# Performance work log

Hardware: AMD Instinct MI355X
Metric: run time of the kernel (lower is better)

Reference implementation:

```python
import jax, jax.numpy as jnp
import numpy as np

# Config (decoder-only Transformer)
NL, H, D, DK, V, B, S = 6, 16, 1024, 64, 32000, 2, 1024  # DK = d_v = D // H
DFF = 4 * D


def _layer_norm(x, g, b, eps=1e-5):
    mu = jnp.mean(x, axis=-1, keepdims=True)
    var = jnp.mean(jnp.square(x - mu), axis=-1, keepdims=True)
    return (x - mu) * jax.lax.rsqrt(var + eps) * g + b


def _pos_encoding(seq_len, d_embed):
    # Matches PositionalEncoding: base 1000 (as in source), sin at even i, cos at odd i
    pos = jnp.arange(seq_len, dtype=jnp.float32)[:, None]
    i = jnp.arange(d_embed, dtype=jnp.float32)[None, :]
    angle = pos / jnp.power(1000.0, i / d_embed)
    return jnp.where((jnp.arange(d_embed)[None, :] % 2) == 0, jnp.sin(angle), jnp.cos(angle))


def setup_inputs() -> dict:
    key = jax.random.key(0)
    ks = jax.random.split(key, 8)
    n = lambda k, shp, sc: jax.random.normal(k, shp, dtype=jnp.float32) * sc
    return {
        "outputs": jax.random.randint(ks[0], (B, S), 0, V),
        "embed": n(ks[1], (V, D), 0.02),
        # per-head Q/K/V projections stacked over layers and heads: [NL, H, D, DK]
        "Wq": n(ks[2], (NL, H, D, DK), D ** -0.5),
        "Wk": n(ks[3], (NL, H, D, DK), D ** -0.5),
        "Wv": n(ks[4], (NL, H, D, DK), D ** -0.5),
        "W1": n(ks[5], (NL, D, DFF), D ** -0.5),
        "W2": n(ks[6], (NL, DFF, D), DFF ** -0.5),
        "ln1_g": jnp.ones((NL, D), jnp.float32),
        "ln1_b": jnp.zeros((NL, D), jnp.float32),
        "ln2_g": jnp.ones((NL, D), jnp.float32),
        "ln2_b": jnp.zeros((NL, D), jnp.float32),
        "Wout": n(ks[7], (D, V), D ** -0.5),
        "bout": jnp.zeros((V,), jnp.float32),
    }


def reference(outputs, embed, Wq, Wk, Wv, W1, W2, ln1_g, ln1_b, ln2_g, ln2_b, Wout, bout):
    x = embed[outputs]                      # [B, S, D]
    x = x + _pos_encoding(S, D)
    scale = jnp.float32(DK ** 0.5)
    for l in range(NL):
        # Masked multi-head self-attention (per-head projections batched over H)
        q = jnp.einsum('bsd,hdk->bhsk', x, Wq[l])
        k = jnp.einsum('bsd,hdk->bhsk', x, Wk[l])
        v = jnp.einsum('bsd,hdk->bhsk', x, Wv[l])
        scores = jnp.einsum('bhqk,bhsk->bhqs', q, k) / scale   # [B,H,S,S]
        # Faithful to source: tril then masked_fill(score == 0, -inf)
        scores = jnp.tril(scores)
        scores = jnp.where(scores == 0, -jnp.inf, scores)
        w = jax.nn.softmax(scores, axis=-1)
        attn = jnp.einsum('bhqs,bhsv->bqhv', w, v).reshape(B, S, H * DK)
        x = _layer_norm(x + attn, ln1_g[l], ln1_b[l])
        # Position-wise FFN (dropout is identity at inference)
        h = jax.nn.relu(x @ W1[l]) @ W2[l]
        x = _layer_norm(x + h, ln2_g[l], ln2_b[l])
    return x @ Wout + bout                  # logits [B, S, V]
```

## Files before the change

### kernel.cpp

```cpp
#include <hip/hip_runtime.h>

typedef unsigned short u16;
typedef __attribute__((ext_vector_type(8))) short short8;
typedef __attribute__((ext_vector_type(4))) short short4_t;
typedef __attribute__((ext_vector_type(4))) float f32x4;

#define NLAYER 6
#define NH 16
#define DMODEL 1024
#define DHEAD 64
#define NVOCAB 32000
#define NB 2
#define NS 1024
#define NDFF 4096
#define MTOK (NB*NS)

__device__ __forceinline__ u16 f2b(float f) {
    union { float f; unsigned u; } x; x.f = f;
    unsigned r = x.u + 0x7fffu + ((x.u >> 16) & 1u);
    return (u16)(r >> 16);
}

#define GLL16(gp, lp) __builtin_amdgcn_global_load_lds( \
    (const __attribute__((address_space(1))) void*)(gp), \
    (__attribute__((address_space(3))) void*)(lp), 16, 0, 0)

__global__ __launch_bounds__(256) void trans64(
    const float* __restrict__ src, u16* __restrict__ dst,
    int R, int C, long sStride, long dStride)
{
    __shared__ float sh[64][65];
    const int c0 = blockIdx.x * 64, r0 = blockIdx.y * 64;
    const float* s = src + (long)blockIdx.z * sStride;
    u16* d = dst + (long)blockIdx.z * dStride;
    const int tid = threadIdx.x;
    const int lr = tid >> 4, lc = (tid & 15) * 4;
    #pragma unroll
    for (int q = 0; q < 4; ++q) {
        const float4 v = *(const float4*)(s + (long)(r0 + q * 16 + lr) * C + c0 + lc);
        sh[q * 16 + lr][lc + 0] = v.x;
        sh[q * 16 + lr][lc + 1] = v.y;
        sh[q * 16 + lr][lc + 2] = v.z;
        sh[q * 16 + lr][lc + 3] = v.w;
    }
    __syncthreads();
    #pragma unroll
    for (int k = 0; k < 2; ++k) {
        const int t = tid + 256 * k;
        const int col = t >> 3, rch = (t & 7) * 8;
        u16 tmp[8];
        #pragma unroll
        for (int j = 0; j < 8; ++j) tmp[j] = f2b(sh[rch + j][col]);
        *(short8*)(d + (long)(c0 + col) * R + r0 + rch) = *(const short8*)tmp;
    }
}

__global__ void transpose_qkv(const float* __restrict__ src, u16* __restrict__ dst, int sel)
{
    __shared__ float t[32][33];
    const int bi = blockIdx.z, l = bi >> 4, h = bi & 15;
    const float* s = src + (long)bi * (DMODEL * DHEAD);
    u16* d = dst + (long)l * 3072 * DMODEL + (long)(sel * 1024 + h * 64) * DMODEL;
    const int c0 = blockIdx.x * 32, r0 = blockIdx.y * 32;
    const int tx = threadIdx.x, ty = threadIdx.y;
    #pragma unroll
    for (int j = 0; j < 32; j += 8)
        t[ty + j][tx] = s[(long)(r0 + ty + j) * DHEAD + c0 + tx];
    __syncthreads();
    #pragma unroll
    for (int j = 0; j < 32; j += 8)
        d[(long)(c0 + ty + j) * DMODEL + r0 + tx] = f2b(t[tx][ty + j]);
}

__global__ void embed_pe(const int* __restrict__ toks, const float* __restrict__ emb,
                         float* __restrict__ x, u16* __restrict__ xb)
{
    const int row = blockIdx.x;
    const int s = row & (NS - 1);
    const long erow = (long)toks[row] * DMODEL;
    const long base = (long)row * DMODEL;
    #pragma unroll
    for (int j = 0; j < 4; ++j) {
        int d = threadIdx.x + j * 256;
        float ang = (float)s * exp2f(-(float)d * (9.965784284662087f / 1024.f));
        float pe = (d & 1) ? cosf(ang) : sinf(ang);
        float v = emb[erow + d] + pe;
        x[base + d] = v;
        xb[base + d] = f2b(v);
    }
}

template<int ND>
__global__ __launch_bounds__(256) void ln_residual(
    const float* __restrict__ xin, const float* __restrict__ delta, size_t pstride,
    const float* __restrict__ g, const float* __restrict__ bb,
    float* __restrict__ xout, u16* __restrict__ xbout)
{
    __shared__ float red[8];
    const long base = (long)blockIdx.x * DMODEL;
    const int d = threadIdx.x * 4;
    f32x4 v = *(const f32x4*)(xin + base + d);
    #pragma unroll
    for (int y = 0; y < ND; ++y)
        v += *(const f32x4*)(delta + base + (size_t)y * pstride + d);
    float sum = v[0] + v[1] + v[2] + v[3];
    float sq  = v[0]*v[0] + v[1]*v[1] + v[2]*v[2] + v[3]*v[3];
    #pragma unroll
    for (int off = 1; off < 64; off <<= 1) {
        sum += __shfl_xor(sum, off, 64);
        sq  += __shfl_xor(sq,  off, 64);
    }
    const int wv = threadIdx.x >> 6, lane = threadIdx.x & 63;
    if (lane == 0) { red[wv] = sum; red[4 + wv] = sq; }
    __syncthreads();
    float ts = red[0] + red[1] + red[2] + red[3];
    float tq = red[4] + red[5] + red[6] + red[7];
    float mu = ts * (1.f / DMODEL);
    float var = tq * (1.f / DMODEL) - mu * mu;
    float rstd = rsqrtf(var + 1e-5f);
    const f32x4 gg = *(const f32x4*)(g + d);
    const f32x4 bv = *(const f32x4*)(bb + d);
    f32x4 yv = (v - mu) * rstd * gg + bv;
    *(f32x4*)(xout + base + d) = yv;
    u16 fourv[4];
    #pragma unroll
    for (int i = 0; i < 4; ++i) fourv[i] = f2b(yv[i]);
    *(short4_t*)(xbout + base + d) = *(const short4_t*)fourv;
}

template<int BM, int EPI>
__global__ __launch_bounds__(BM*2, 2) void gemm_pipe(
    const u16* __restrict__ A, const u16* __restrict__ Bt,
    void* __restrict__ Cout, const float* __restrict__ bias,
    int M, int N, int K, int lda, int ldb, size_t zstride)
{
    constexpr int WAVES = BM / 32;
    constexpr int WC = WAVES / 2;
    constexpr int MR = BM / 32;
    constexpr int TILE = BM * 32;

    __shared__ __align__(16) u16 As[4][TILE];
    __shared__ __align__(16) u16 Bs[4][TILE];

    const int nmb = M / BM;
    const int id = blockIdx.x, nwg = gridDim.x;
    const int q = nwg >> 3, r = nwg & 7, xcd = id & 7, loc = id >> 3;
    const int swz = (xcd < r ? xcd * (q + 1) : r * (q + 1) + (xcd - r) * q) + loc;
    const int m0 = (swz % nmb) * BM, n0 = (swz / nmb) * BM;
    const int koff = blockIdx.y * K;

    const int tid = threadIdx.x, wv = tid >> 6, lane = tid & 63;
    const int wr = wv / WC, wc = wv % WC;
    const int lrow = lane & 15, ks = lane >> 4;

    const u16* gsrc[4];
    int ldso[2];
    {
        const int l4 = lane >> 2, s = lane & 3;
        #pragma unroll
        for (int j = 0; j < 2; ++j) {
            const int row = j * (WAVES * 16) + wv * 16 + l4;
            const int x = (row >> 1) & 3;
            gsrc[j]     = A  + (size_t)(m0 + row) * lda + koff + (size_t)((s ^ x) * 8);
            gsrc[2 + j] = Bt + (size_t)(n0 + row) * ldb + koff + (size_t)((s ^ x) * 8);
            ldso[j] = (j * (WAVES * 16) + wv * 16) * 32;
        }
    }
    int aoff[MR], boff[4];
    #pragma unroll
    for (int m = 0; m < MR; ++m) {
        const int row = wr * (BM / 2) + m * 16 + lrow;
        aoff[m] = row * 32 + ((ks ^ ((row >> 1) & 3)) * 8);
    }
    #pragma unroll
    for (int n = 0; n < 4; ++n) {
        const int row = wc * 64 + n * 16 + lrow;
        boff[n] = row * 32 + ((ks ^ ((row >> 1) & 3)) * 8);
    }

    const int NT = K / 32;
    auto ISSUE = [&](int t) {
        const int b = t & 3;
        const size_t ko = (size_t)t * 32;
        #pragma unroll
        for (int j = 0; j < 2; ++j) {
            GLL16(gsrc[j] + ko,     &As[b][ldso[j]]);
            GLL16(gsrc[2 + j] + ko, &Bs[b][ldso[j]]);
        }
    };

    f32x4 acc[MR][4] = {};
    ISSUE(0); ISSUE(1); ISSUE(2);

    for (int t = 0; t < NT; ++t) {
        if (t < NT - 2)       { asm volatile("s_waitcnt vmcnt(8)" ::: "memory"); }
        else if (t == NT - 2) { asm volatile("s_waitcnt vmcnt(4)" ::: "memory"); }
        else                  { asm volatile("s_waitcnt vmcnt(0)" ::: "memory"); }
        __builtin_amdgcn_sched_barrier(0);
        __builtin_amdgcn_s_barrier();
        __builtin_amdgcn_sched_barrier(0);

        const int b = t & 3;
        short8 af[MR], bf[4];
        #pragma unroll
        for (int m = 0; m < MR; ++m) af[m] = *(const short8*)(&As[b][aoff[m]]);
        #pragma unroll
        for (int n = 0; n < 4; ++n)  bf[n] = *(const short8*)(&Bs[b][boff[n]]);
        if (t + 3 < NT) ISSUE(t + 3);
        __builtin_amdgcn_s_setprio(1);
        #pragma unroll
        for (int m = 0; m < MR; ++m)
            #pragma unroll
            for (int n = 0; n < 4; ++n)
                acc[m][n] = __builtin_amdgcn_mfma_f32_16x16x32_bf16(af[m], bf[n], acc[m][n], 0, 0, 0);
        __builtin_amdgcn_s_setprio(0);
    }

    if (EPI == 0 || EPI == 3) {
        __syncthreads();
        float* patch = (float*)((WAVES == 8 && (wv & 4)) ? (void*)&Bs[0][0] : (void*)&As[0][0])
                       + (wv & 3) * (16 * 68);
        const int cc0 = n0 + wc * 64;
        f32x4 bvv = {};
        if (EPI == 3) bvv = *(const f32x4*)(bias + cc0 + (lane & 15) * 4);
        float* C = (float*)Cout + (EPI == 0 ? (size_t)blockIdx.y * zstride : (size_t)0);
        #pragma unroll
        for (int m = 0; m < MR; ++m) {
            #pragma unroll
            for (int n = 0; n < 4; ++n)
                #pragma unroll
                for (int i = 0; i < 4; ++i)
                    patch[(ks * 4 + i) * 68 + n * 16 + lrow] = acc[m][n][i];
            #pragma unroll
            for (int i2 = 0; i2 < 4; ++i2) {
                const int prow = i2 * 4 + ks;
                f32x4 v = *(const f32x4*)(patch + prow * 68 + (lane & 15) * 4);
                if (EPI == 3) v += bvv;
                const int rr = m0 + wr * (BM / 2) + m * 16 + prow;
                *(f32x4*)(C + (size_t)rr * N + cc0 + (lane & 15) * 4) = v;
            }
        }
    } else {
        u16* C = (u16*)Cout;
        #pragma unroll
        for (int m = 0; m < MR; ++m) {
            const int rr = m0 + wr * (BM / 2) + m * 16 + ks * 4;
            #pragma unroll
            for (int n = 0; n < 4; ++n) {
                const int cc = n0 + wc * 64 + n * 16 + lrow;
                #pragma unroll
                for (int i = 0; i < 4; ++i) {
                    float vv = acc[m][n][i];
                    if (EPI == 2) vv = fmaxf(vv, 0.f);
                    C[(size_t)(rr + i) * N + cc] = f2b(vv);
                }
            }
        }
    }
}

__global__ __launch_bounds__(256, 2) void attn_flash4(
    const u16* __restrict__ qk, const u16* __restrict__ vT, float* __restrict__ delta)
{
    __shared__ __align__(16) u16 Qs[64 * 64];
    __shared__ __align__(16) u16 Kd[2][64 * 64];
    __shared__ __align__(16) u16 Vd[2][64 * 64];
    __shared__ __align__(16) u16 Ps[4][16 * 64];

    const int pair = blockIdx.x, h = blockIdx.y, b = blockIdx.z;
    const int tid = threadIdx.x, wv = tid >> 6, lane = tid & 63;
    const int lrow = lane & 15, ks4 = lane >> 4, li4 = ks4 * 4;
    const long baseQK = (long)b * NS * 2048;
    const u16* vbase = vT + (long)h * 64 * 2048 + b * NS;
    u16* ps = &Ps[wv][0];

    for (int rep = 0; rep < 2; ++rep) {
        const int qt = rep ? 15 - pair : pair;
        __syncthreads();

        #pragma unroll
        for (int i = 0; i < 2; ++i) {
            const int c = (wv * 2 + i) * 64 + lane;
            const int row = c >> 3, u = (c & 7) ^ (row & 7);
            GLL16(qk + baseQK + (long)(qt * 64 + row) * 2048 + h * 64 + u * 8, Qs + c * 8);
            GLL16(qk + baseQK + (long)row * 2048 + 1024 + h * 64 + u * 8, Kd[0] + c * 8);
            GLL16(vbase + (long)row * 2048 + u * 8, Vd[0] + c * 8);
        }
        __syncthreads();

        short8 aq[2];
        {
            const int row = wv * 16 + lrow;
            aq[0] = *(const short8*)(Qs + row * 64 + ((ks4 ^ (row & 7)) * 8));
            aq[1] = *(const short8*)(Qs + row * 64 + (((4 + ks4) ^ (row & 7)) * 8));
        }

        f32x4 o[4] = {};
        float m_ = -__builtin_inff(), l_ = 0.f;

        for (int t = 0; t <= qt; ++t) {
            const int p = t & 1;
            if (t < qt) {
                #pragma unroll
                for (int i = 0; i < 2; ++i) {
                    const int c = (wv * 2 + i) * 64 + lane;
                    const int row = c >> 3, u = (c & 7) ^ (row & 7);
                    GLL16(qk + baseQK + (long)((t + 1) * 64 + row) * 2048 + 1024 + h * 64 + u * 8, Kd[p ^ 1] + c * 8);
                    GLL16(vbase + (long)row * 2048 + (t + 1) * 64 + u * 8, Vd[p ^ 1] + c * 8);
                }
            }
            f32x4 sa[4];
            #pragma unroll
            for (int nb = 0; nb < 4; ++nb) {
                f32x4 z = {};
                #pragma unroll
                for (int kd = 0; kd < 2; ++kd) {
                    const int row = nb * 16 + lrow;
                    short8 bk = *(const short8*)(Kd[p] + row * 64 + (((kd * 4 + ks4) ^ (row & 7)) * 8));
                    z = __builtin_amdgcn_mfma_f32_16x16x32_bf16(bk, aq[kd], z, 0, 0, 0);
                }
                sa[nb] = z;
            }
            const int qg = qt * 64 + wv * 16 + lrow;
            #pragma unroll
            for (int nb = 0; nb < 4; ++nb)
                #pragma unroll
                for (int i = 0; i < 4; ++i) {
                    float sc = sa[nb][i] * 0.125f;
                    if (t == qt && (t * 64 + nb * 16 + li4 + i) > qg) sc = -__builtin_inff();
                    sa[nb][i] = sc;
                }
            float mt = sa[0][0];
            #pragma unroll
            for (int nb = 0; nb < 4; ++nb)
                #pragma unroll
                for (int i = 0; i < 4; ++i) mt = fmaxf(mt, sa[nb][i]);
            mt = fmaxf(mt, __shfl_xor(mt, 16, 64));
            mt = fmaxf(mt, __shfl_xor(mt, 32, 64));
            const float mn = fmaxf(m_, mt);
            const float fac = expf(m_ - mn);
            m_ = mn;
            float rs = 0.f;
            #pragma unroll
            for (int nb = 0; nb < 4; ++nb)
                #pragma unroll
                for (int i = 0; i < 4; ++i) {
                    float pp = expf(sa[nb][i] - mn);
                    sa[nb][i] = pp; rs += pp;
                }
            rs += __shfl_xor(rs, 16, 64);
            rs += __shfl_xor(rs, 32, 64);
            l_ = l_ * fac + rs;
            #pragma unroll
            for (int nd = 0; nd < 4; ++nd) o[nd] *= fac;

            #pragma unroll
            for (int nb = 0; nb < 4; ++nb) {
                u16 fourv[4];
                #pragma unroll
                for (int i = 0; i < 4; ++i) fourv[i] = f2b(sa[nb][i]);
                const int kvb = nb * 16 + li4;
                const int addr = lrow * 64 + (((kvb >> 3) ^ (lrow & 7)) * 8) + (kvb & 7);
                *(short4_t*)(ps + addr) = *(const short4_t*)fourv;
            }
            short8 pa[2];
            pa[0] = *(const short8*)(ps + lrow * 64 + ((ks4 ^ (lrow & 7)) * 8));
            pa[1] = *(const short8*)(ps + lrow * 64 + (((4 + ks4) ^ (lrow & 7)) * 8));
            #pragma unroll
            for (int nd = 0; nd < 4; ++nd)
                #pragma unroll
                for (int kd = 0; kd < 2; ++kd) {
                    const int row = nd * 16 + lrow;
                    short8 vb = *(const short8*)(Vd[p] + row * 64 + (((kd * 4 + ks4) ^ (row & 7)) * 8));
                    o[nd] = __builtin_amdgcn_mfma_f32_16x16x32_bf16(vb, pa[kd], o[nd], 0, 0, 0);
                }
            __syncthreads();
        }

        const float inv = 1.f / l_;
        const long tok = (long)b * NS + qt * 64 + wv * 16 + lrow;
        #pragma unroll
        for (int nd = 0; nd < 4; ++nd) {
            f32x4 v = o[nd] * inv;
            *(f32x4*)(delta + tok * DMODEL + h * 64 + nd * 16 + li4) = v;
        }
    }
}

extern "C" void kernel_launch(void* const* d_in, const int* in_sizes, int n_in,
                              void* d_out, int out_size, void* d_ws, size_t ws_size,
                              hipStream_t stream) {
    const int*   toks  = (const int*)d_in[0];
    const float* emb   = (const float*)d_in[1];
    const float* Wq    = (const float*)d_in[2];
    const float* Wk    = (const float*)d_in[3];
    const float* Wv    = (const float*)d_in[4];
    const float* W1    = (const float*)d_in[5];
    const float* W2    = (const float*)d_in[6];
    const float* ln1g  = (const float*)d_in[7];
    const float* ln1b  = (const float*)d_in[8];
    const float* ln2g  = (const float*)d_in[9];
    const float* ln2b  = (const float*)d_in[10];
    const float* Wout  = (const float*)d_in[11];
    const float* bout  = (const float*)d_in[12];

    char* p = (char*)d_ws;
    auto alloc = [&](size_t bytes) { void* r = (void*)p; p += (bytes + 255) & ~(size_t)255; return r; };
    const size_t PSZ = (size_t)MTOK * 1024;
    u16*   Wqkv_t = (u16*)alloc((size_t)NLAYER * 3072 * 1024 * 2);
    u16*   W1t    = (u16*)alloc((size_t)NLAYER * 4096 * 1024 * 2);
    u16*   W2t    = (u16*)alloc((size_t)NLAYER * 1024 * 4096 * 2);
    u16*   Woutt  = (u16*)alloc((size_t)NVOCAB * 1024 * 2);
    float* x      = (float*)alloc((size_t)MTOK * 1024 * 4);
    u16*   xb     = (u16*)alloc((size_t)MTOK * 1024 * 2);
    u16*   qkbuf  = (u16*)alloc((size_t)MTOK * 2048 * 2);
    u16*   vTbuf  = (u16*)alloc((size_t)1024 * MTOK * 2);
    u16*   hbuf   = (u16*)alloc((size_t)MTOK * 4096 * 2);
    float* dbuf   = (float*)alloc(PSZ * 4 * 4);

    float* hbufF = (float*)hbuf;

    transpose_qkv<<<dim3(2, 32, 96), dim3(32, 8), 0, stream>>>(Wq, Wqkv_t, 0);
    transpose_qkv<<<dim3(2, 32, 96), dim3(32, 8), 0, stream>>>(Wk, Wqkv_t, 1);
    transpose_qkv<<<dim3(2, 32, 96), dim3(32, 8), 0, stream>>>(Wv, Wqkv_t, 2);
    trans64<<<dim3(64, 16, 6), 256, 0, stream>>>(W1, W1t, 1024, 4096, 1024l * 4096, 4096l * 1024);
    trans64<<<dim3(16, 64, 6), 256, 0, stream>>>(W2, W2t, 4096, 1024, 4096l * 1024, 1024l * 4096);
    trans64<<<dim3(500, 16, 1), 256, 0, stream>>>(Wout, Woutt, 1024, NVOCAB, 0, 0);

    embed_pe<<<MTOK, 256, 0, stream>>>(toks, emb, x, xb);

    for (int l = 0; l < NLAYER; ++l) {
        const u16* Wl = Wqkv_t + (size_t)l * 3072 * 1024;
        gemm_pipe<128, 1><<<dim3(16 * 16), 256, 0, stream>>>(
            xb, Wl, qkbuf, nullptr, MTOK, 2048, 1024, 1024, 1024, 0);
        gemm_pipe<128, 1><<<dim3(8 * 16), 256, 0, stream>>>(
            Wl + (size_t)2048 * 1024, xb, vTbuf, nullptr, 1024, MTOK, 1024, 1024, 1024, 0);
        attn_flash4<<<dim3(8, NH, NB), 256, 0, stream>>>(qkbuf, vTbuf, hbufF);
        ln_residual<1><<<MTOK, 256, 0, stream>>>(x, hbufF, 0,
            ln1g + l * 1024, ln1b + l * 1024, x, xb);
        gemm_pipe<128, 2><<<dim3(16 * 32), 256, 0, stream>>>(
            xb, W1t + (size_t)l * 4096 * 1024, hbuf, nullptr, MTOK, 4096, 1024, 1024, 1024, 0);
        gemm_pipe<128, 0><<<dim3(16 * 8, 4), 256, 0, stream>>>(
            hbuf, W2t + (size_t)l * 1024 * 4096, dbuf, nullptr, MTOK, 1024, 1024, 4096, 4096, PSZ);
        ln_residual<4><<<MTOK, 256, 0, stream>>>(x, dbuf, PSZ,
            ln2g + l * 1024, ln2b + l * 1024, x, xb);
    }

    gemm_pipe<256, 3><<<dim3(8 * 125), 512, 0, stream>>>(
        xb, Woutt, (float*)d_out, bout, MTOK, NVOCAB, 1024, 1024, 1024, 0);
}
```

Baseline: 1.158 ms.

## Switch GEMM MFMA to 32x32x16 tiles and halve W2 split-K partials

The pipelined GEMM now issues 32x32x16 bf16 MFMA instructions instead of 16x16x32 ones, with new LDS fragment offsets and rewritten epilogue index mappings for the 16-element accumulators. This is meant to cut LDS fragment reads per MFMA and raise matrix-core efficiency. Separately, the FFN down-projection split-K factor drops from 4 to 2, which halves the partial-sum buffer traffic and the reduction work in the following layernorm. The cost is fewer workgroups for that GEMM, so occupancy is lower there.

```diff
diff --git a/kernel.cpp b/kernel.cpp
--- a/kernel.cpp
+++ b/kernel.cpp
@@ -4,6 +4,7 @@
 typedef __attribute__((ext_vector_type(8))) short short8;
 typedef __attribute__((ext_vector_type(4))) short short4_t;
 typedef __attribute__((ext_vector_type(4))) float f32x4;
+typedef __attribute__((ext_vector_type(16))) float f32x16;
 
 #define NLAYER 6
 #define NH 16
@@ -136,7 +137,7 @@
 {
     constexpr int WAVES = BM / 32;
     constexpr int WC = WAVES / 2;
-    constexpr int MR = BM / 32;
+    constexpr int MT = (BM / 2) / 32;
     constexpr int TILE = BM * 32;
 
     __shared__ __align__(16) u16 As[4][TILE];
@@ -151,7 +152,7 @@
 
     const int tid = threadIdx.x, wv = tid >> 6, lane = tid & 63;
     const int wr = wv / WC, wc = wv % WC;
-    const int lrow = lane & 15, ks = lane >> 4;
+    const int l31 = lane & 31, kh = lane >> 5;
 
     const u16* gsrc[4];
     int ldso[2];
@@ -166,17 +167,21 @@
             ldso[j] = (j * (WAVES * 16) + wv * 16) * 32;
         }
     }
-    int aoff[MR], boff[4];
-    #pragma unroll
-    for (int m = 0; m < MR; ++m) {
-        const int row = wr * (BM / 2) + m * 16 + lrow;
-        aoff[m] = row * 32 + ((ks ^ ((row >> 1) & 3)) * 8);
-    }
-    #pragma unroll
-    for (int n = 0; n < 4; ++n) {
-        const int row = wc * 64 + n * 16 + lrow;
-        boff[n] = row * 32 + ((ks ^ ((row >> 1) & 3)) * 8);
-    }
+    int aoff[MT][2], boff[2][2];
+    #pragma unroll
+    for (int mt = 0; mt < MT; ++mt)
+        #pragma unroll
+        for (int kk = 0; kk < 2; ++kk) {
+            const int row = wr * (BM / 2) + mt * 32 + l31;
+            aoff[mt][kk] = row * 32 + (((kk * 2 + kh) ^ ((row >> 1) & 3)) * 8);
+        }
+    #pragma unroll
+    for (int nt = 0; nt < 2; ++nt)
+        #pragma unroll
+        for (int kk = 0; kk < 2; ++kk) {
+            const int row = wc * 64 + nt * 32 + l31;
+            boff[nt][kk] = row * 32 + (((kk * 2 + kh) ^ ((row >> 1) & 3)) * 8);
+        }
 
     const int NT = K / 32;
     auto ISSUE = [&](int t) {
@@ -189,7 +194,7 @@
         }
     };
 
-    f32x4 acc[MR][4] = {};
+    f32x16 acc[MT][2] = {};
     ISSUE(0); ISSUE(1); ISSUE(2);
 
     for (int t = 0; t < NT; ++t) {
@@ -201,58 +206,65 @@
         __builtin_amdgcn_sched_barrier(0);
 
         const int b = t & 3;
-        short8 af[MR], bf[4];
-        #pragma unroll
-        for (int m = 0; m < MR; ++m) af[m] = *(const short8*)(&As[b][aoff[m]]);
-        #pragma unroll
-        for (int n = 0; n < 4; ++n)  bf[n] = *(const short8*)(&Bs[b][boff[n]]);
+        short8 af[MT][2], bf[2][2];
+        #pragma unroll
+        for (int mt = 0; mt < MT; ++mt)
+            #pragma unroll
+            for (int kk = 0; kk < 2; ++kk) af[mt][kk] = *(const short8*)(&As[b][aoff[mt][kk]]);
+        #pragma unroll
+        for (int nt = 0; nt < 2; ++nt)
+            #pragma unroll
+            for (int kk = 0; kk < 2; ++kk) bf[nt][kk] = *(const short8*)(&Bs[b][boff[nt][kk]]);
         if (t + 3 < NT) ISSUE(t + 3);
         __builtin_amdgcn_s_setprio(1);
         #pragma unroll
-        for (int m = 0; m < MR; ++m)
-            #pragma unroll
-            for (int n = 0; n < 4; ++n)
-                acc[m][n] = __builtin_amdgcn_mfma_f32_16x16x32_bf16(af[m], bf[n], acc[m][n], 0, 0, 0);
+        for (int mt = 0; mt < MT; ++mt)
+            #pragma unroll
+            for (int nt = 0; nt < 2; ++nt)
+                #pragma unroll
+                for (int kk = 0; kk < 2; ++kk)
+                    acc[mt][nt] = __builtin_amdgcn_mfma_f32_32x32x16_bf16(
+                        af[mt][kk], bf[nt][kk], acc[mt][nt], 0, 0, 0);
         __builtin_amdgcn_s_setprio(0);
     }
 
     if (EPI == 0 || EPI == 3) {
         __syncthreads();
-        float* patch = (float*)((WAVES == 8 && (wv & 4)) ? (void*)&Bs[0][0] : (void*)&As[0][0])
-                       + (wv & 3) * (16 * 68);
+        float* patch = (float*)((wv & WC) ? (void*)&Bs[0][0] : (void*)&As[0][0])
+                       + (wv & (WC - 1)) * (32 * 68);
+        float* C = (float*)Cout + (EPI == 0 ? (size_t)blockIdx.y * zstride : (size_t)0);
         const int cc0 = n0 + wc * 64;
         f32x4 bvv = {};
         if (EPI == 3) bvv = *(const f32x4*)(bias + cc0 + (lane & 15) * 4);
-        float* C = (float*)Cout + (EPI == 0 ? (size_t)blockIdx.y * zstride : (size_t)0);
-        #pragma unroll
-        for (int m = 0; m < MR; ++m) {
-            #pragma unroll
-            for (int n = 0; n < 4; ++n)
-                #pragma unroll
-                for (int i = 0; i < 4; ++i)
-                    patch[(ks * 4 + i) * 68 + n * 16 + lrow] = acc[m][n][i];
-            #pragma unroll
-            for (int i2 = 0; i2 < 4; ++i2) {
-                const int prow = i2 * 4 + ks;
+        #pragma unroll
+        for (int mt = 0; mt < MT; ++mt) {
+            #pragma unroll
+            for (int nt = 0; nt < 2; ++nt)
+                #pragma unroll
+                for (int rg = 0; rg < 16; ++rg)
+                    patch[((rg & 3) + 8 * (rg >> 2) + 4 * kh) * 68 + nt * 32 + l31] = acc[mt][nt][rg];
+            #pragma unroll
+            for (int i2 = 0; i2 < 8; ++i2) {
+                const int prow = i2 * 4 + (lane >> 4);
                 f32x4 v = *(const f32x4*)(patch + prow * 68 + (lane & 15) * 4);
                 if (EPI == 3) v += bvv;
-                const int rr = m0 + wr * (BM / 2) + m * 16 + prow;
+                const int rr = m0 + wr * (BM / 2) + mt * 32 + prow;
                 *(f32x4*)(C + (size_t)rr * N + cc0 + (lane & 15) * 4) = v;
             }
         }
     } else {
         u16* C = (u16*)Cout;
         #pragma unroll
-        for (int m = 0; m < MR; ++m) {
-            const int rr = m0 + wr * (BM / 2) + m * 16 + ks * 4;
-            #pragma unroll
-            for (int n = 0; n < 4; ++n) {
-                const int cc = n0 + wc * 64 + n * 16 + lrow;
-                #pragma unroll
-                for (int i = 0; i < 4; ++i) {
-                    float vv = acc[m][n][i];
+        for (int mt = 0; mt < MT; ++mt) {
+            const int rbase = m0 + wr * (BM / 2) + mt * 32 + 4 * kh;
+            #pragma unroll
+            for (int nt = 0; nt < 2; ++nt) {
+                const int cc = n0 + wc * 64 + nt * 32 + l31;
+                #pragma unroll
+                for (int rg = 0; rg < 16; ++rg) {
+                    float vv = acc[mt][nt][rg];
                     if (EPI == 2) vv = fmaxf(vv, 0.f);
-                    C[(size_t)(rr + i) * N + cc] = f2b(vv);
+                    C[(size_t)(rbase + (rg & 3) + 8 * (rg >> 2)) * N + cc] = f2b(vv);
                 }
             }
         }
@@ -416,7 +428,7 @@
     u16*   qkbuf  = (u16*)alloc((size_t)MTOK * 2048 * 2);
     u16*   vTbuf  = (u16*)alloc((size_t)1024 * MTOK * 2);
     u16*   hbuf   = (u16*)alloc((size_t)MTOK * 4096 * 2);
-    float* dbuf   = (float*)alloc(PSZ * 4 * 4);
+    float* dbuf   = (float*)alloc(PSZ * 2 * 4);
 
     float* hbufF = (float*)hbuf;
 
@@ -440,9 +452,9 @@
             ln1g + l * 1024, ln1b + l * 1024, x, xb);
         gemm_pipe<128, 2><<<dim3(16 * 32), 256, 0, stream>>>(
             xb, W1t + (size_t)l * 4096 * 1024, hbuf, nullptr, MTOK, 4096, 1024, 1024, 1024, 0);
-        gemm_pipe<128, 0><<<dim3(16 * 8, 4), 256, 0, stream>>>(
-            hbuf, W2t + (size_t)l * 1024 * 4096, dbuf, nullptr, MTOK, 1024, 1024, 4096, 4096, PSZ);
-        ln_residual<4><<<MTOK, 256, 0, stream>>>(x, dbuf, PSZ,
+        gemm_pipe<128, 0><<<dim3(16 * 8, 2), 256, 0, stream>>>(
+            hbuf, W2t + (size_t)l * 1024 * 4096, dbuf, nullptr, MTOK, 1024, 2048, 4096, 4096, PSZ);
+        ln_residual<2><<<MTOK, 256, 0, stream>>>(x, dbuf, PSZ,
             ln2g + l * 1024, ln2b + l * 1024, x, xb);
     }
 
```

Result: slower. 1.194 ms (+3.2%).

## Add 8-phase pipelined 256x256 GEMM for output projection; halve FFN2 split-K

Applied to the files above, without the earlier changes.

Adds a new gemm8p kernel for the vocab projection. It uses 256x256 tiles, XCD-aware block swizzling, and a double-buffered LDS pipeline that interleaves global-to-LDS loads with four MFMA phases per k-tile, using setprio and explicit waitcnt control. Separately, the FFN down-projection split-K goes from 4 to 2 partials, which cuts partial-sum traffic and the reduction work in ln_residual at the cost of fewer workgroups. The new kernel's hand-tuned barrier and wait scheduling is fragile and raises register and LDS pressure.

```diff
diff --git a/kernel.cpp b/kernel.cpp
--- a/kernel.cpp
+++ b/kernel.cpp
@@ -255,6 +255,163 @@
                     C[(size_t)(rr + i) * N + cc] = f2b(vv);
                 }
             }
+        }
+    }
+}
+
+__global__ __launch_bounds__(512, 2) void gemm8p(
+    const u16* __restrict__ A, const u16* __restrict__ Bt,
+    float* __restrict__ C, const float* __restrict__ bias,
+    int M, int N, int K)
+{
+    __shared__ __align__(16) u16 As[2][2][128 * 64];
+    __shared__ __align__(16) u16 Bs[2][2][128 * 64];
+
+    const int nmb = M >> 8;
+    const int id = blockIdx.x, nwg = gridDim.x;
+    const int q = nwg >> 3, r = nwg & 7, xcd = id & 7, loc = id >> 3;
+    const int swz = (xcd < r ? xcd * (q + 1) : r * (q + 1) + (xcd - r) * q) + loc;
+    const int m0 = (swz % nmb) * 256, n0 = (swz / nmb) * 256;
+
+    const int tid = threadIdx.x, wv = tid >> 6, lane = tid & 63;
+    const int wr = wv >> 2, wc = wv & 3, bh = wc >> 1;
+    const int lrow = lane & 15, ks4 = lane >> 4;
+
+    const u16* sA[2][2]; const u16* sB[2][2]; int dso[2];
+    #pragma unroll
+    for (int i = 0; i < 2; ++i) {
+        const int c = tid + i * 512, row = c >> 3, pp = c & 7;
+        const int uc = (pp ^ (row & 7)) * 8;
+        #pragma unroll
+        for (int h = 0; h < 2; ++h) {
+            sA[i][h] = A  + (size_t)(m0 + h * 128 + row) * K + uc;
+            sB[i][h] = Bt + (size_t)(n0 + h * 128 + row) * K + uc;
+        }
+        dso[i] = c * 8;
+    }
+    int aoff[8][2], boff[4][2];
+    #pragma unroll
+    for (int m = 0; m < 8; ++m) {
+        const int hr = m * 16 + lrow;
+        #pragma unroll
+        for (int kk = 0; kk < 2; ++kk)
+            aoff[m][kk] = hr * 64 + (((kk * 4 + ks4) ^ (hr & 7)) * 8);
+    }
+    #pragma unroll
+    for (int n = 0; n < 4; ++n) {
+        const int hr = (wc & 1) * 64 + n * 16 + lrow;
+        #pragma unroll
+        for (int kk = 0; kk < 2; ++kk)
+            boff[n][kk] = hr * 64 + (((kk * 4 + ks4) ^ (hr & 7)) * 8);
+    }
+
+    auto SA_ = [&](int t, int h) {
+        const int s = t & 1; const size_t ko = (size_t)t * 64;
+        #pragma unroll
+        for (int i = 0; i < 2; ++i) GLL16(sA[i][h] + ko, &As[s][h][dso[i]]);
+    };
+    auto SB_ = [&](int t, int h) {
+        const int s = t & 1; const size_t ko = (size_t)t * 64;
+        #pragma unroll
+        for (int i = 0; i < 2; ++i) GLL16(sB[i][h] + ko, &Bs[s][h][dso[i]]);
+    };
+
+    const int NT = K >> 6;
+    SB_(0, 0); SB_(0, 1); SA_(0, 0); SA_(0, 1); SB_(1, 0);
+
+    f32x4 acc[8][4] = {};
+    short8 af[4], bf[4];
+
+    for (int t = 0; t < NT; ++t) {
+        const int s = t & 1;
+        if (t < NT - 1) { asm volatile("s_waitcnt vmcnt(2)" ::: "memory"); }
+        else            { asm volatile("s_waitcnt vmcnt(0)" ::: "memory"); }
+        __builtin_amdgcn_sched_barrier(0);
+        __builtin_amdgcn_s_barrier();
+        __builtin_amdgcn_sched_barrier(0);
+
+        #pragma unroll
+        for (int m = 0; m < 4; ++m) af[m] = *(const short8*)(&As[s][wr][aoff[m][0]]);
+        #pragma unroll
+        for (int n = 0; n < 4; ++n) bf[n] = *(const short8*)(&Bs[s][bh][boff[n][0]]);
+        if (t + 1 < NT) SB_(t + 1, 1);
+        __builtin_amdgcn_s_barrier();
+        asm volatile("s_waitcnt lgkmcnt(0)" ::: "memory");
+        __builtin_amdgcn_sched_barrier(0);
+        __builtin_amdgcn_s_setprio(1);
+        #pragma unroll
+        for (int m = 0; m < 4; ++m)
+            #pragma unroll
+            for (int n = 0; n < 4; ++n)
+                acc[m][n] = __builtin_amdgcn_mfma_f32_16x16x32_bf16(af[m], bf[n], acc[m][n], 0, 0, 0);
+        __builtin_amdgcn_s_setprio(0);
+        __builtin_amdgcn_s_barrier();
+
+        #pragma unroll
+        for (int m = 0; m < 4; ++m) af[m] = *(const short8*)(&As[s][wr][aoff[4 + m][0]]);
+        if (t + 1 < NT) SA_(t + 1, 0);
+        __builtin_amdgcn_s_barrier();
+        asm volatile("s_waitcnt lgkmcnt(0)" ::: "memory");
+        __builtin_amdgcn_sched_barrier(0);
+        __builtin_amdgcn_s_setprio(1);
+        #pragma unroll
+        for (int m = 0; m < 4; ++m)
+            #pragma unroll
+            for (int n = 0; n < 4; ++n)
+                acc[4 + m][n] = __builtin_amdgcn_mfma_f32_16x16x32_bf16(af[m], bf[n], acc[4 + m][n], 0, 0, 0);
+        __builtin_amdgcn_s_setprio(0);
+        __builtin_amdgcn_s_barrier();
+
+        #pragma unroll
+        for (int m = 0; m < 4; ++m) af[m] = *(const short8*)(&As[s][wr][aoff[m][1]]);
+        #pragma unroll
+        for (int n = 0; n < 4; ++n) bf[n] = *(const short8*)(&Bs[s][bh][boff[n][1]]);
+        if (t + 1 < NT) SA_(t + 1, 1);
+        __builtin_amdgcn_s_barrier();
+        asm volatile("s_waitcnt lgkmcnt(0)" ::: "memory");
+        __builtin_amdgcn_sched_barrier(0);
+        __builtin_amdgcn_s_setprio(1);
+        #pragma unroll
+        for (int m = 0; m < 4; ++m)
+            #pragma unroll
+            for (int n = 0; n < 4; ++n)
+                acc[m][n] = __builtin_amdgcn_mfma_f32_16x16x32_bf16(af[m], bf[n], acc[m][n], 0, 0, 0);
+        __builtin_amdgcn_s_setprio(0);
+        __builtin_amdgcn_s_barrier();
+
+        #pragma unroll
+        for (int m = 0; m < 4; ++m) af[m] = *(const short8*)(&As[s][wr][aoff[4 + m][1]]);
+        if (t + 2 < NT) SB_(t + 2, 0);
+        __builtin_amdgcn_s_barrier();
+        asm volatile("s_waitcnt lgkmcnt(0)" ::: "memory");
+        __builtin_amdgcn_sched_barrier(0);
+        __builtin_amdgcn_s_setprio(1);
+        #pragma unroll
+        for (int m = 0; m < 4; ++m)
+            #pragma unroll
+            for (int n = 0; n < 4; ++n)
+                acc[4 + m][n] = __builtin_amdgcn_mfma_f32_16x16x32_bf16(af[m], bf[n], acc[4 + m][n], 0, 0, 0);
+        __builtin_amdgcn_s_setprio(0);
+    }
+
+    __syncthreads();
+    float* patch = (float*)((wv & 4) ? (void*)&Bs[0][0][0] : (void*)&As[0][0][0])
+                   + (wv & 3) * (16 * 68);
+    const int cc0 = n0 + wc * 64;
+    const f32x4 bvv = *(const f32x4*)(bias + cc0 + (lane & 15) * 4);
+    #pragma unroll
+    for (int m = 0; m < 8; ++m) {
+        #pragma unroll
+        for (int n = 0; n < 4; ++n)
+            #pragma unroll
+            for (int i = 0; i < 4; ++i)
+                patch[(ks4 * 4 + i) * 68 + n * 16 + lrow] = acc[m][n][i];
+        #pragma unroll
+        for (int i2 = 0; i2 < 4; ++i2) {
+            const int prow = i2 * 4 + ks4;
+            f32x4 v = *(const f32x4*)(patch + prow * 68 + (lane & 15) * 4) + bvv;
+            const int rr = m0 + wr * 128 + m * 16 + prow;
+            *(f32x4*)(C + (size_t)rr * N + cc0 + (lane & 15) * 4) = v;
         }
     }
 }
@@ -416,7 +573,7 @@
     u16*   qkbuf  = (u16*)alloc((size_t)MTOK * 2048 * 2);
     u16*   vTbuf  = (u16*)alloc((size_t)1024 * MTOK * 2);
     u16*   hbuf   = (u16*)alloc((size_t)MTOK * 4096 * 2);
-    float* dbuf   = (float*)alloc(PSZ * 4 * 4);
+    float* dbuf   = (float*)alloc(PSZ * 2 * 4);
 
     float* hbufF = (float*)hbuf;
 
@@ -440,12 +597,12 @@
             ln1g + l * 1024, ln1b + l * 1024, x, xb);
         gemm_pipe<128, 2><<<dim3(16 * 32), 256, 0, stream>>>(
             xb, W1t + (size_t)l * 4096 * 1024, hbuf, nullptr, MTOK, 4096, 1024, 1024, 1024, 0);
-        gemm_pipe<128, 0><<<dim3(16 * 8, 4), 256, 0, stream>>>(
-            hbuf, W2t + (size_t)l * 1024 * 4096, dbuf, nullptr, MTOK, 1024, 1024, 4096, 4096, PSZ);
-        ln_residual<4><<<MTOK, 256, 0, stream>>>(x, dbuf, PSZ,
+        gemm_pipe<128, 0><<<dim3(16 * 8, 2), 256, 0, stream>>>(
+            hbuf, W2t + (size_t)l * 1024 * 4096, dbuf, nullptr, MTOK, 1024, 2048, 4096, 4096, PSZ);
+        ln_residual<2><<<MTOK, 256, 0, stream>>>(x, dbuf, PSZ,
             ln2g + l * 1024, ln2b + l * 1024, x, xb);
     }
 
-    gemm_pipe<256, 3><<<dim3(8 * 125), 512, 0, stream>>>(
-        xb, Woutt, (float*)d_out, bout, MTOK, NVOCAB, 1024, 1024, 1024, 0);
-}
+    gemm8p<<<dim3(1000), 512, 0, stream>>>(
+        xb, Woutt, (float*)d_out, bout, MTOK, NVOCAB, 1024);
+}
```

Measured after the change: 1.210 ms. 4.5% more time.
